# Optimization experiments

Hardware: AMD Instinct MI355X
Metric: run time of the kernel (lower is better)

## Reference

```python
import jax, jax.numpy as jnp
import numpy as np

IN_FEATURES = 4096
OUT_FEATURES = 4096
BLOCK_SIZE = 64
P = 0.1          # fraction of blocks kept
N_TOKENS = 8192


def setup_inputs() -> dict:
    key = jax.random.key(0)
    k_x, k_w, k_m, k_b = jax.random.split(key, 4)
    x = jax.random.normal(k_x, (N_TOKENS, IN_FEATURES), dtype=jnp.float32)
    # kaiming_uniform_(a=sqrt(5)) on [out, in] -> bound = 1/sqrt(in_features)
    bound = 1.0 / np.sqrt(IN_FEATURES)
    weight = jax.random.uniform(k_w, (OUT_FEATURES, IN_FEATURES), dtype=jnp.float32,
                                minval=-bound, maxval=bound)
    bias = jax.random.uniform(k_b, (OUT_FEATURES,), dtype=jnp.float32,
                              minval=-bound, maxval=bound)
    # Block-structured 0/1 mask: keep each BLOCK_SIZE x BLOCK_SIZE block with prob P
    nb_out, nb_in = OUT_FEATURES // BLOCK_SIZE, IN_FEATURES // BLOCK_SIZE
    block_keep = (jax.random.uniform(k_m, (nb_out, nb_in)) < P).astype(jnp.float32)
    mask = jnp.repeat(jnp.repeat(block_keep, BLOCK_SIZE, axis=0), BLOCK_SIZE, axis=1)
    return {"input": x, "weight": weight, "bias": bias, "mask": mask}


def reference(input, weight, bias, mask):
    # bsr_dense_mm((W*mask).to_sparse_bsr(), x.T).T + bias == x @ (W*mask).T + bias
    masked_w = weight * mask                      # [out, in]
    return input @ masked_w.T + bias              # [N, out]
```

## Files before the change

kernel.cpp:

```cpp
#include <hip/hip_runtime.h>
#include <hip/hip_fp16.h>
#include <cstdint>

#define IN_F   4096
#define OUT_F  4096
#define BS     64
#define NB     64
#define N_TOK  8192
#define TM     256
#define BK     64
#define NMT    (N_TOK / TM)

typedef __attribute__((ext_vector_type(8))) _Float16       f16x8;
typedef __attribute__((ext_vector_type(8))) unsigned short u16x8;
typedef __attribute__((ext_vector_type(4))) float          f32x4;

#define WS_XT_OFF      0ull
#define WS_XT_BYTES    (2048ull * 32768ull)
#define WS_WT_OFF      (WS_XT_OFF + WS_XT_BYTES)
#define WS_WT_BYTES    (4096ull * 8192ull)
#define WS_NEEDED      (WS_WT_OFF + WS_WT_BYTES)

__device__ __forceinline__ u16x8 cvt_f16x8(const float* v) {
    u16x8 o;
#pragma unroll
    for (int j = 0; j < 8; ++j)
        o[j] = __half_as_ushort(__float2half_rn(v[j]));
    return o;
}

__device__ __forceinline__ unsigned long long mask_ballot(
        const float* __restrict__ mask, int br, int lane) {
    float mv = mask[(size_t)(br * BS) * IN_F + (size_t)lane * BS];
    return __ballot(mv != 0.0f);
}

__global__ __launch_bounds__(256, 1)
void convert_x_kernel(const float* __restrict__ x, unsigned short* __restrict__ xt) {
    const int t  = blockIdx.x;
    const int mt = t >> 6, kb = t & 63;
    unsigned short* tile = xt + (size_t)t * 16384;

    float4 va[8], vb[8];
#pragma unroll
    for (int l = 0; l < 8; ++l) {
        int g   = threadIdx.x + l * 256;
        int row = g >> 3, slot = g & 7;
        const float* src = x + (size_t)(mt * TM + row) * IN_F + kb * BK + slot * 8;
        va[l] = *(const float4*)src;
        vb[l] = *(const float4*)(src + 4);
    }
#pragma unroll
    for (int l = 0; l < 8; ++l) {
        int g   = threadIdx.x + l * 256;
        int row = g >> 3, slot = g & 7;
        float v[8] = {va[l].x, va[l].y, va[l].z, va[l].w,
                      vb[l].x, vb[l].y, vb[l].z, vb[l].w};
        *(u16x8*)&tile[row * 64 + ((slot ^ (row & 7)) << 3)] = cvt_f16x8(v);
    }
}

__global__ __launch_bounds__(256)
void convert_w_kernel(const float* __restrict__ w,
                      const float* __restrict__ mask,
                      unsigned short* __restrict__ wt) {
    const int br   = blockIdx.y, si = blockIdx.x;
    const int lane = threadIdx.x & 63;
    unsigned long long ball = mask_ballot(mask, br, lane);
    if (si >= __popcll(ball)) return;
    bool fl = ((ball >> lane) & 1ull) &&
              (__popcll(ball & ((1ull << lane) - 1ull)) == si);
    unsigned long long m2 = __ballot(fl);
    const int kb = __ffsll(m2) - 1;
    unsigned short* tile = wt + (size_t)(br * NB + si) * 4096;

    float4 va[2], vb[2];
#pragma unroll
    for (int l = 0; l < 2; ++l) {
        int g   = threadIdx.x + l * 256;
        int row = g >> 3, slot = g & 7;
        const float* src = w + (size_t)(br * BS + row) * IN_F + kb * BK + slot * 8;
        va[l] = *(const float4*)src;
        vb[l] = *(const float4*)(src + 4);
    }
#pragma unroll
    for (int l = 0; l < 2; ++l) {
        int g   = threadIdx.x + l * 256;
        int row = g >> 3, slot = g & 7;
        float v[8] = {va[l].x, va[l].y, va[l].z, va[l].w,
                      vb[l].x, vb[l].y, vb[l].z, vb[l].w};
        *(u16x8*)&tile[row * 64 + ((slot ^ (row & 7)) << 3)] = cvt_f16x8(v);
    }
}

__device__ __forceinline__ void gll16(const void* g, void* l) {
    __builtin_amdgcn_global_load_lds(
        (const __attribute__((address_space(1))) unsigned int*)g,
        (__attribute__((address_space(3))) unsigned int*)l, 16, 0, 0);
}

__global__ __launch_bounds__(256, 2)
void bsr_mfma5_kernel(const unsigned short* __restrict__ xt,
                      const unsigned short* __restrict__ wt,
                      const float* __restrict__ bias,
                      const float* __restrict__ mask,
                      float* __restrict__ out) {
    __shared__ unsigned short xs[2][TM * BK];
    __shared__ unsigned short wsb[2][BS * BK];

    const int b     = blockIdx.x;
    const int xcd   = b & 7;
    const int j     = b >> 3;
    const int phase = j >> 7;
    const int idx   = j & 127;
    const int br    = idx >> 1;
    const int mt    = xcd * 4 + phase * 2 + (idx & 1);

    const int tid  = threadIdx.x;
    const int lane = tid & 63;
    const int wv   = tid >> 6;
    const int fr   = lane & 15;
    const int kg   = lane >> 4;

    unsigned long long ball = mask_ballot(mask, br, lane);
    const int cnt = __popcll(ball);

    f32x4 acc[4][4];
#pragma unroll
    for (int a = 0; a < 4; ++a)
#pragma unroll
        for (int c = 0; c < 4; ++c) acc[a][c] = (f32x4)0.0f;

    const char* xbase = (const char*)xt;
    const char* wbase = (const char*)wt;

    auto stage = [&](int kb, int si, int bb) {
        const char* xg = xbase + ((size_t)(mt * 64 + kb) << 15);
        const char* wg = wbase + ((size_t)(br * 64 + si) << 13);
        const int bx = wv * 8192;
#pragma unroll
        for (int q = 0; q < 8; ++q)
            gll16(xg + bx + q * 1024 + lane * 16, (char*)xs[bb] + bx + q * 1024);
        const int bw = wv * 2048;
#pragma unroll
        for (int q = 0; q < 2; ++q)
            gll16(wg + bw + q * 1024 + lane * 16, (char*)wsb[bb] + bw + q * 1024);
    };

    unsigned long long rem = ball;
    int cur = 0;
    if (cnt > 0) {
        int kb0 = __ffsll(rem) - 1;
        rem &= rem - 1;
        stage(kb0, 0, 0);
    }
    __syncthreads();

    for (int si = 0; si < cnt; ++si) {
        if (si + 1 < cnt) {
            int kbn = __ffsll(rem) - 1;
            rem &= rem - 1;
            stage(kbn, si + 1, cur ^ 1);
        }

#pragma unroll
        for (int ks = 0; ks < 2; ++ks) {
            f16x8 a[4], bfr[4];
#pragma unroll
            for (int mr = 0; mr < 4; ++mr) {
                int row = wv * 64 + mr * 16 + fr;
                a[mr] = *(const f16x8*)&xs[cur][row * 64 + (((ks * 4 + kg) ^ (row & 7)) << 3)];
            }
#pragma unroll
            for (int nr = 0; nr < 4; ++nr) {
                int row = nr * 16 + fr;
                bfr[nr] = *(const f16x8*)&wsb[cur][row * 64 + (((ks * 4 + kg) ^ (row & 7)) << 3)];
            }
#pragma unroll
            for (int mr = 0; mr < 4; ++mr)
#pragma unroll
                for (int nr = 0; nr < 4; ++nr)
                    acc[mr][nr] = __builtin_amdgcn_mfma_f32_16x16x32_f16(
                        a[mr], bfr[nr], acc[mr][nr], 0, 0, 0);
        }
        __syncthreads();
        cur ^= 1;
    }

    const int mbase = mt * TM;
    const int obase = br * BS;
#pragma unroll
    for (int nr = 0; nr < 4; ++nr) {
        float bv = bias[obase + nr * 16 + fr];
#pragma unroll
        for (int mr = 0; mr < 4; ++mr) {
#pragma unroll
            for (int r = 0; r < 4; ++r) {
                int m = mbase + wv * 64 + mr * 16 + kg * 4 + r;
                out[(size_t)m * OUT_F + obase + nr * 16 + fr] = acc[mr][nr][r] + bv;
            }
        }
    }
}

__global__ __launch_bounds__(256, 3)
void bsr_fused_kernel(const float* __restrict__ x,
                      const float* __restrict__ w,
                      const float* __restrict__ bias,
                      const float* __restrict__ mask,
                      float* __restrict__ out) {
    __shared__ unsigned short xs[128 * BK];
    __shared__ unsigned short wsb[BS * BK];

    const int mt   = blockIdx.x;
    const int br   = blockIdx.y;
    const int tid  = threadIdx.x;
    const int lane = tid & 63;
    const int wv   = tid >> 6;
    const int fr   = lane & 15;
    const int kg   = lane >> 4;

    const int mbase = mt * 128;
    const int obase = br * BS;

    unsigned long long ball = mask_ballot(mask, br, lane);
    const int cnt = __popcll(ball);
    unsigned long long rem = ball;

    f32x4 acc[2][4];
#pragma unroll
    for (int a = 0; a < 2; ++a)
#pragma unroll
        for (int c = 0; c < 4; ++c) acc[a][c] = (f32x4)0.0f;

    for (int si = 0; si < cnt; ++si) {
        const int kb = __ffsll(rem) - 1;
        rem &= rem - 1;
        const int kbase = kb * BS;
#pragma unroll
        for (int l = 0; l < 4; ++l) {
            int g = tid + l * 256;
            int row = g >> 3, slot = g & 7;
            const float* src = x + (size_t)(mbase + row) * IN_F + kbase + slot * 8;
            float4 v0 = *(const float4*)src;
            float4 v1 = *(const float4*)(src + 4);
            float v[8] = {v0.x, v0.y, v0.z, v0.w, v1.x, v1.y, v1.z, v1.w};
            *(u16x8*)&xs[row * BK + ((slot ^ (row & 7)) << 3)] = cvt_f16x8(v);
        }
#pragma unroll
        for (int l = 0; l < 2; ++l) {
            int g = tid + l * 256;
            int row = g >> 3, slot = g & 7;
            const float* src = w + (size_t)(obase + row) * IN_F + kbase + slot * 8;
            float4 v0 = *(const float4*)src;
            float4 v1 = *(const float4*)(src + 4);
            float v[8] = {v0.x, v0.y, v0.z, v0.w, v1.x, v1.y, v1.z, v1.w};
            *(u16x8*)&wsb[row * BK + ((slot ^ (row & 7)) << 3)] = cvt_f16x8(v);
        }
        __syncthreads();
#pragma unroll
        for (int ks = 0; ks < 2; ++ks) {
            f16x8 a[2], bfr[4];
#pragma unroll
            for (int mr = 0; mr < 2; ++mr) {
                int row = wv * 32 + mr * 16 + fr;
                a[mr] = *(const f16x8*)&xs[row * BK + (((ks * 4 + kg) ^ (row & 7)) << 3)];
            }
#pragma unroll
            for (int nr = 0; nr < 4; ++nr) {
                int row = nr * 16 + fr;
                bfr[nr] = *(const f16x8*)&wsb[row * BK + (((ks * 4 + kg) ^ (row & 7)) << 3)];
            }
#pragma unroll
            for (int mr = 0; mr < 2; ++mr)
#pragma unroll
                for (int nr = 0; nr < 4; ++nr)
                    acc[mr][nr] = __builtin_amdgcn_mfma_f32_16x16x32_f16(
                        a[mr], bfr[nr], acc[mr][nr], 0, 0, 0);
        }
        __syncthreads();
    }

#pragma unroll
    for (int nr = 0; nr < 4; ++nr) {
        float bv = bias[obase + nr * 16 + fr];
#pragma unroll
        for (int mr = 0; mr < 2; ++mr) {
#pragma unroll
            for (int r = 0; r < 4; ++r) {
                int m = mbase + wv * 32 + mr * 16 + kg * 4 + r;
                out[(size_t)m * OUT_F + obase + nr * 16 + fr] = acc[mr][nr][r] + bv;
            }
        }
    }
}

extern "C" void kernel_launch(void* const* d_in, const int* in_sizes, int n_in,
                              void* d_out, int out_size, void* d_ws, size_t ws_size,
                              hipStream_t stream) {
    const float* x    = (const float*)d_in[0];
    const float* w    = (const float*)d_in[1];
    const float* bias = (const float*)d_in[2];
    const float* mask = (const float*)d_in[3];
    float* out = (float*)d_out;

    if (ws_size >= WS_NEEDED) {
        unsigned short* xt = (unsigned short*)((char*)d_ws + WS_XT_OFF);
        unsigned short* wt = (unsigned short*)((char*)d_ws + WS_WT_OFF);
        convert_x_kernel<<<2048, 256, 0, stream>>>(x, xt);
        convert_w_kernel<<<dim3(NB, NB), 256, 0, stream>>>(w, mask, wt);
        bsr_mfma5_kernel<<<NMT * NB, 256, 0, stream>>>(xt, wt, bias, mask, out);
    } else {
        dim3 grid(N_TOK / 128, NB);
        bsr_fused_kernel<<<grid, 256, 0, stream>>>(x, w, bias, mask, out);
    }
}
```

Before: 116.4 us.

## Fuse x fp16 conversion into BSR matmul, loading operands directly into registers

Drops the separate pass that converts x to a swizzled fp16 copy in workspace. The matmul kernel now reads fp32 x straight from global memory into registers, converts it to fp16 and feeds MFMA, with the pre-converted weight tiles also read directly from global memory. This removes LDS staging and all barriers, and uses 512-thread blocks of eight waves, each wave owning 32 rows. The aim is to avoid writing and re-reading a 64MB intermediate. In exchange x is read in fp32 with less coalesced per-lane row access, global loads are no longer explicitly double-buffered, and each x tile is converted again for every output block row.

Measured after the change: 175.3 us. +50.6%, slower.

```diff
diff --git a/kernel.cpp b/kernel.cpp
--- a/kernel.cpp
+++ b/kernel.cpp
@@ -8,26 +8,14 @@
 #define NB     64
 #define N_TOK  8192
 #define TM     256
-#define BK     64
 #define NMT    (N_TOK / TM)
 
 typedef __attribute__((ext_vector_type(8))) _Float16       f16x8;
 typedef __attribute__((ext_vector_type(8))) unsigned short u16x8;
 typedef __attribute__((ext_vector_type(4))) float          f32x4;
 
-#define WS_XT_OFF      0ull
-#define WS_XT_BYTES    (2048ull * 32768ull)
-#define WS_WT_OFF      (WS_XT_OFF + WS_XT_BYTES)
 #define WS_WT_BYTES    (4096ull * 8192ull)
-#define WS_NEEDED      (WS_WT_OFF + WS_WT_BYTES)
-
-__device__ __forceinline__ u16x8 cvt_f16x8(const float* v) {
-    u16x8 o;
-#pragma unroll
-    for (int j = 0; j < 8; ++j)
-        o[j] = __half_as_ushort(__float2half_rn(v[j]));
-    return o;
-}
+#define WS_NEEDED      WS_WT_BYTES
 
 __device__ __forceinline__ unsigned long long mask_ballot(
         const float* __restrict__ mask, int br, int lane) {
@@ -35,29 +23,13 @@
     return __ballot(mv != 0.0f);
 }
 
-__global__ __launch_bounds__(256, 1)
-void convert_x_kernel(const float* __restrict__ x, unsigned short* __restrict__ xt) {
-    const int t  = blockIdx.x;
-    const int mt = t >> 6, kb = t & 63;
-    unsigned short* tile = xt + (size_t)t * 16384;
-
-    float4 va[8], vb[8];
-#pragma unroll
-    for (int l = 0; l < 8; ++l) {
-        int g   = threadIdx.x + l * 256;
-        int row = g >> 3, slot = g & 7;
-        const float* src = x + (size_t)(mt * TM + row) * IN_F + kb * BK + slot * 8;
-        va[l] = *(const float4*)src;
-        vb[l] = *(const float4*)(src + 4);
-    }
-#pragma unroll
-    for (int l = 0; l < 8; ++l) {
-        int g   = threadIdx.x + l * 256;
-        int row = g >> 3, slot = g & 7;
-        float v[8] = {va[l].x, va[l].y, va[l].z, va[l].w,
-                      vb[l].x, vb[l].y, vb[l].z, vb[l].w};
-        *(u16x8*)&tile[row * 64 + ((slot ^ (row & 7)) << 3)] = cvt_f16x8(v);
-    }
+__device__ __forceinline__ u16x8 pack8(f32x4 a, f32x4 b) {
+    u16x8 o;
+#pragma unroll
+    for (int j = 0; j < 4; ++j) o[j]     = __half_as_ushort(__float2half_rn(a[j]));
+#pragma unroll
+    for (int j = 0; j < 4; ++j) o[4 + j] = __half_as_ushort(__float2half_rn(b[j]));
+    return o;
 }
 
 __global__ __launch_bounds__(256)
@@ -79,7 +51,7 @@
     for (int l = 0; l < 2; ++l) {
         int g   = threadIdx.x + l * 256;
         int row = g >> 3, slot = g & 7;
-        const float* src = w + (size_t)(br * BS + row) * IN_F + kb * BK + slot * 8;
+        const float* src = w + (size_t)(br * BS + row) * IN_F + kb * BS + slot * 8;
         va[l] = *(const float4*)src;
         vb[l] = *(const float4*)(src + 4);
     }
@@ -87,34 +59,23 @@
     for (int l = 0; l < 2; ++l) {
         int g   = threadIdx.x + l * 256;
         int row = g >> 3, slot = g & 7;
-        float v[8] = {va[l].x, va[l].y, va[l].z, va[l].w,
-                      vb[l].x, vb[l].y, vb[l].z, vb[l].w};
-        *(u16x8*)&tile[row * 64 + ((slot ^ (row & 7)) << 3)] = cvt_f16x8(v);
-    }
-}
-
-__device__ __forceinline__ void gll16(const void* g, void* l) {
-    __builtin_amdgcn_global_load_lds(
-        (const __attribute__((address_space(1))) unsigned int*)g,
-        (__attribute__((address_space(3))) unsigned int*)l, 16, 0, 0);
-}
-
-__global__ __launch_bounds__(256, 2)
-void bsr_mfma5_kernel(const unsigned short* __restrict__ xt,
-                      const unsigned short* __restrict__ wt,
-                      const float* __restrict__ bias,
-                      const float* __restrict__ mask,
-                      float* __restrict__ out) {
-    __shared__ unsigned short xs[2][TM * BK];
-    __shared__ unsigned short wsb[2][BS * BK];
-
+        u16x8 p = pack8(*(f32x4*)&va[l], *(f32x4*)&vb[l]);
+        *(u16x8*)&tile[row * 64 + ((slot ^ (row & 7)) << 3)] = p;
+    }
+}
+
+__global__ __launch_bounds__(512, 4)
+void bsr_fused3_kernel(const float* __restrict__ x,
+                       const unsigned short* __restrict__ wt,
+                       const float* __restrict__ bias,
+                       const float* __restrict__ mask,
+                       float* __restrict__ out) {
     const int b     = blockIdx.x;
     const int xcd   = b & 7;
     const int j     = b >> 3;
-    const int phase = j >> 7;
-    const int idx   = j & 127;
-    const int br    = idx >> 1;
-    const int mt    = xcd * 4 + phase * 2 + (idx & 1);
+    const int phase = j >> 6;
+    const int br    = j & 63;
+    const int mt    = xcd * 4 + phase;
 
     const int tid  = threadIdx.x;
     const int lane = tid & 63;
@@ -122,81 +83,67 @@
     const int fr   = lane & 15;
     const int kg   = lane >> 4;
 
+    const int mbase = mt * TM;
+    const int obase = br * BS;
+
     unsigned long long ball = mask_ballot(mask, br, lane);
     const int cnt = __popcll(ball);
 
-    f32x4 acc[4][4];
-#pragma unroll
-    for (int a = 0; a < 4; ++a)
+    f32x4 acc[2][4];
+#pragma unroll
+    for (int a = 0; a < 2; ++a)
 #pragma unroll
         for (int c = 0; c < 4; ++c) acc[a][c] = (f32x4)0.0f;
 
-    const char* xbase = (const char*)xt;
-    const char* wbase = (const char*)wt;
-
-    auto stage = [&](int kb, int si, int bb) {
-        const char* xg = xbase + ((size_t)(mt * 64 + kb) << 15);
-        const char* wg = wbase + ((size_t)(br * 64 + si) << 13);
-        const int bx = wv * 8192;
-#pragma unroll
-        for (int q = 0; q < 8; ++q)
-            gll16(xg + bx + q * 1024 + lane * 16, (char*)xs[bb] + bx + q * 1024);
-        const int bw = wv * 2048;
-#pragma unroll
-        for (int q = 0; q < 2; ++q)
-            gll16(wg + bw + q * 1024 + lane * 16, (char*)wsb[bb] + bw + q * 1024);
-    };
+    const unsigned short* wbr = wt + (size_t)br * NB * 4096;
+    const float* xw = x + (size_t)mbase * IN_F;
 
     unsigned long long rem = ball;
-    int cur = 0;
-    if (cnt > 0) {
-        int kb0 = __ffsll(rem) - 1;
+    for (int si = 0; si < cnt; ++si) {
+        const int kb = __ffsll(rem) - 1;
         rem &= rem - 1;
-        stage(kb0, 0, 0);
-    }
-    __syncthreads();
-
-    for (int si = 0; si < cnt; ++si) {
-        if (si + 1 < cnt) {
-            int kbn = __ffsll(rem) - 1;
-            rem &= rem - 1;
-            stage(kbn, si + 1, cur ^ 1);
-        }
-
-#pragma unroll
-        for (int ks = 0; ks < 2; ++ks) {
-            f16x8 a[4], bfr[4];
-#pragma unroll
-            for (int mr = 0; mr < 4; ++mr) {
-                int row = wv * 64 + mr * 16 + fr;
-                a[mr] = *(const f16x8*)&xs[cur][row * 64 + (((ks * 4 + kg) ^ (row & 7)) << 3)];
-            }
+
+        f32x4 ra[4][2];
+#pragma unroll
+        for (int mr = 0; mr < 2; ++mr)
+#pragma unroll
+            for (int ks = 0; ks < 2; ++ks) {
+                const f32x4* src = (const f32x4*)(xw
+                    + (size_t)(wv * 32 + mr * 16 + fr) * IN_F
+                    + kb * BS + ks * 32 + kg * 8);
+                ra[mr * 2 + ks][0] = src[0];
+                ra[mr * 2 + ks][1] = src[1];
+            }
+        f16x8 bq[2][4];
+#pragma unroll
+        for (int ks = 0; ks < 2; ++ks)
 #pragma unroll
             for (int nr = 0; nr < 4; ++nr) {
                 int row = nr * 16 + fr;
-                bfr[nr] = *(const f16x8*)&wsb[cur][row * 64 + (((ks * 4 + kg) ^ (row & 7)) << 3)];
-            }
-#pragma unroll
-            for (int mr = 0; mr < 4; ++mr)
+                bq[ks][nr] = *(const f16x8*)&wbr[(size_t)si * 4096
+                    + row * 64 + (((ks * 4 + kg) ^ (row & 7)) << 3)];
+            }
+#pragma unroll
+        for (int ks = 0; ks < 2; ++ks)
+#pragma unroll
+            for (int mr = 0; mr < 2; ++mr) {
+                u16x8 t = pack8(ra[mr * 2 + ks][0], ra[mr * 2 + ks][1]);
+                f16x8 af = *(f16x8*)&t;
 #pragma unroll
                 for (int nr = 0; nr < 4; ++nr)
                     acc[mr][nr] = __builtin_amdgcn_mfma_f32_16x16x32_f16(
-                        a[mr], bfr[nr], acc[mr][nr], 0, 0, 0);
-        }
-        __syncthreads();
-        cur ^= 1;
-    }
-
-    const int mbase = mt * TM;
-    const int obase = br * BS;
+                        af, bq[ks][nr], acc[mr][nr], 0, 0, 0);
+            }
+    }
+
 #pragma unroll
     for (int nr = 0; nr < 4; ++nr) {
         float bv = bias[obase + nr * 16 + fr];
 #pragma unroll
-        for (int mr = 0; mr < 4; ++mr) {
+        for (int mr = 0; mr < 2; ++mr) {
 #pragma unroll
             for (int r = 0; r < 4; ++r) {
-                int m = mbase + wv * 64 + mr * 16 + kg * 4 + r;
+                int m = mbase + wv * 32 + mr * 16 + kg * 4 + r;
                 out[(size_t)m * OUT_F + obase + nr * 16 + fr] = acc[mr][nr][r] + bv;
             }
         }
@@ -209,8 +156,8 @@
                       const float* __restrict__ bias,
                       const float* __restrict__ mask,
                       float* __restrict__ out) {
-    __shared__ unsigned short xs[128 * BK];
-    __shared__ unsigned short wsb[BS * BK];
+    __shared__ unsigned short xs[128 * BS];
+    __shared__ unsigned short wsb[BS * BS];
 
     const int mt   = blockIdx.x;
     const int br   = blockIdx.y;
@@ -242,20 +189,18 @@
             int g = tid + l * 256;
             int row = g >> 3, slot = g & 7;
             const float* src = x + (size_t)(mbase + row) * IN_F + kbase + slot * 8;
-            float4 v0 = *(const float4*)src;
-            float4 v1 = *(const float4*)(src + 4);
-            float v[8] = {v0.x, v0.y, v0.z, v0.w, v1.x, v1.y, v1.z, v1.w};
-            *(u16x8*)&xs[row * BK + ((slot ^ (row & 7)) << 3)] = cvt_f16x8(v);
+            f32x4 v0 = *(const f32x4*)src;
+            f32x4 v1 = *(const f32x4*)(src + 4);
+            *(u16x8*)&xs[row * BS + ((slot ^ (row & 7)) << 3)] = pack8(v0, v1);
         }
 #pragma unroll
         for (int l = 0; l < 2; ++l) {
             int g = tid + l * 256;
             int row = g >> 3, slot = g & 7;
             const float* src = w + (size_t)(obase + row) * IN_F + kbase + slot * 8;
-            float4 v0 = *(const float4*)src;
-            float4 v1 = *(const float4*)(src + 4);
-            float v[8] = {v0.x, v0.y, v0.z, v0.w, v1.x, v1.y, v1.z, v1.w};
-            *(u16x8*)&wsb[row * BK + ((slot ^ (row & 7)) << 3)] = cvt_f16x8(v);
+            f32x4 v0 = *(const f32x4*)src;
+            f32x4 v1 = *(const f32x4*)(src + 4);
+            *(u16x8*)&wsb[row * BS + ((slot ^ (row & 7)) << 3)] = pack8(v0, v1);
         }
         __syncthreads();
 #pragma unroll
@@ -264,12 +209,12 @@
 #pragma unroll
             for (int mr = 0; mr < 2; ++mr) {
                 int row = wv * 32 + mr * 16 + fr;
-                a[mr] = *(const f16x8*)&xs[row * BK + (((ks * 4 + kg) ^ (row & 7)) << 3)];
+                a[mr] = *(const f16x8*)&xs[row * BS + (((ks * 4 + kg) ^ (row & 7)) << 3)];
             }
 #pragma unroll
             for (int nr = 0; nr < 4; ++nr) {
                 int row = nr * 16 + fr;
-                bfr[nr] = *(const f16x8*)&wsb[row * BK + (((ks * 4 + kg) ^ (row & 7)) << 3)];
+                bfr[nr] = *(const f16x8*)&wsb[row * BS + (((ks * 4 + kg) ^ (row & 7)) << 3)];
             }
 #pragma unroll
             for (int mr = 0; mr < 2; ++mr)
@@ -305,11 +250,9 @@
     float* out = (float*)d_out;
 
     if (ws_size >= WS_NEEDED) {
-        unsigned short* xt = (unsigned short*)((char*)d_ws + WS_XT_OFF);
-        unsigned short* wt = (unsigned short*)((char*)d_ws + WS_WT_OFF);
-        convert_x_kernel<<<2048, 256, 0, stream>>>(x, xt);
+        unsigned short* wt = (unsigned short*)d_ws;
         convert_w_kernel<<<dim3(NB, NB), 256, 0, stream>>>(w, mask, wt);
-        bsr_mfma5_kernel<<<NMT * NB, 256, 0, stream>>>(xt, wt, bias, mask, out);
+        bsr_fused3_kernel<<<NMT * NB, 512, 0, stream>>>(x, wt, bias, mask, out);
     } else {
         dim3 grid(N_TOK / 128, NB);
         bsr_fused_kernel<<<grid, 256, 0, stream>>>(x, w, bias, mask, out);
```
